# Kernel tuning notes

Hardware: AMD Instinct MI355X
Metric: run time of the kernel (lower is better)

## Reference

```python
import jax, jax.numpy as jnp
import numpy as np

EMB = 512
HEADS = 8
HEAD_DIM = EMB // HEADS


def setup_inputs() -> dict:
    key = jax.random.key(0)
    ks = jax.random.split(key, 9)
    s = 1.0 / np.sqrt(EMB)
    return {
        "x": jax.random.normal(ks[0], (4, 2048, EMB), dtype=jnp.float32),
        "Wq": jax.random.uniform(ks[1], (EMB, EMB), jnp.float32, -s, s),
        "bq": jax.random.uniform(ks[2], (EMB,), jnp.float32, -s, s),
        "Wk": jax.random.uniform(ks[3], (EMB, EMB), jnp.float32, -s, s),
        "bk": jax.random.uniform(ks[4], (EMB,), jnp.float32, -s, s),
        "Wv": jax.random.uniform(ks[5], (EMB, EMB), jnp.float32, -s, s),
        "bv": jax.random.uniform(ks[6], (EMB,), jnp.float32, -s, s),
        "Wp": jax.random.uniform(ks[7], (EMB, EMB), jnp.float32, -s, s),
        "bp": jax.random.uniform(ks[8], (EMB,), jnp.float32, -s, s),
    }


def _split_heads(t):
    b, n, _ = t.shape
    return t.reshape(b, n, HEADS, HEAD_DIM).transpose(0, 2, 1, 3)  # b h n d


def reference(x, Wq, bq, Wk, bk, Wv, bv, Wp, bp):
    q = _split_heads(x @ Wq.T + bq)
    k = _split_heads(x @ Wk.T + bk)
    v = _split_heads(x @ Wv.T + bv)
    energy = jnp.einsum("bhqd,bhkd->bhqk", q, k)
    # NOTE: original applies softmax to UNSCALED logits, then divides probs by sqrt(emb)
    att = jax.nn.softmax(energy, axis=-1) / jnp.sqrt(jnp.float32(EMB))
    out = jnp.einsum("bhqk,bhkd->bhqd", att, v)
    b, h, n, d = out.shape
    out = out.transpose(0, 2, 1, 3).reshape(b, n, h * d)
    return out @ Wp.T + bp
```

## Files before the change

kernel.cpp:

```cpp
#include <hip/hip_runtime.h>
#include <math.h>
#include <stdint.h>

#define SEQ  2048
#define LOG2E 1.4426950408889634f

typedef __attribute__((ext_vector_type(4))) float f32x4;
typedef __attribute__((ext_vector_type(16))) float f32x16;
typedef __attribute__((ext_vector_type(8))) short bf16x8;

template <int V> struct IC { static constexpr int value = V; };

__device__ __forceinline__ unsigned packbf(float a, float b) {
    return __builtin_amdgcn_perm(__float_as_uint(b) + 0x8000u,
                                 __float_as_uint(a) + 0x8000u, 0x07060302u);
}

__global__ __launch_bounds__(256, 3) void qkv_kernel(
    const float* __restrict__ xf, const float* __restrict__ wqf,
    const float* __restrict__ wkf, const float* __restrict__ wvf,
    const float* __restrict__ bq, const float* __restrict__ bk,
    const float* __restrict__ bv,
    unsigned short* __restrict__ Qw, unsigned short* __restrict__ Kw,
    unsigned short* __restrict__ VTw)
{
    __shared__ __align__(16) unsigned short smem[8192];
    unsigned short* As = smem;
    unsigned short* Bs = smem + 4096;

    const int t = threadIdx.x;
    const int w = t >> 6, lane = t & 63, quad = (t >> 4) & 3, l15 = t & 15;
    const int wr = w >> 1, wc = w & 1;
    const int m0 = blockIdx.y * 128;
    const int n0 = blockIdx.x * 128;
    const int which = n0 >> 9;
    const float* wbase = which == 0 ? wqf : (which == 1 ? wkf : wvf);
    const int nrow = n0 & 511;

    const int ar = t >> 2, akq = t & 3;
    const float* ax = xf + (size_t)(m0 + ar) * 512 + akq * 8;
    const float* bx = wbase + (size_t)(nrow + ar) * 512 + akq * 8;
    const int lws = (ar & 15) | (akq << 4);
    const int off0 = (ar >> 4) * 512 + lws * 8;
    const int off1 = off0 + 4 * 512;

    f32x4 acc[4][4];
#pragma unroll
    for (int mt = 0; mt < 4; ++mt)
#pragma unroll
        for (int nt = 0; nt < 4; ++nt) acc[mt][nt] = (f32x4){0.f, 0.f, 0.f, 0.f};

    float4 ra[4], rb[4];
    auto loadt = [&](int k0) {
        ra[0] = *(const float4*)(ax + k0);
        ra[1] = *(const float4*)(ax + k0 + 4);
        ra[2] = *(const float4*)(ax + 32768 + k0);
        ra[3] = *(const float4*)(ax + 32768 + k0 + 4);
        rb[0] = *(const float4*)(bx + k0);
        rb[1] = *(const float4*)(bx + k0 + 4);
        rb[2] = *(const float4*)(bx + 32768 + k0);
        rb[3] = *(const float4*)(bx + 32768 + k0 + 4);
    };
    auto writet = [&]() {
        uint4 p;
        p.x = packbf(ra[0].x, ra[0].y); p.y = packbf(ra[0].z, ra[0].w);
        p.z = packbf(ra[1].x, ra[1].y); p.w = packbf(ra[1].z, ra[1].w);
        *(uint4*)(As + off0) = p;
        p.x = packbf(ra[2].x, ra[2].y); p.y = packbf(ra[2].z, ra[2].w);
        p.z = packbf(ra[3].x, ra[3].y); p.w = packbf(ra[3].z, ra[3].w);
        *(uint4*)(As + off1) = p;
        p.x = packbf(rb[0].x, rb[0].y); p.y = packbf(rb[0].z, rb[0].w);
        p.z = packbf(rb[1].x, rb[1].y); p.w = packbf(rb[1].z, rb[1].w);
        *(uint4*)(Bs + off0) = p;
        p.x = packbf(rb[2].x, rb[2].y); p.y = packbf(rb[2].z, rb[2].w);
        p.z = packbf(rb[3].x, rb[3].y); p.w = packbf(rb[3].z, rb[3].w);
        *(uint4*)(Bs + off1) = p;
    };

    loadt(0);
    auto kloop = [&](auto TRC) {
        constexpr int TR = decltype(TRC)::value;
        for (int ki = 0; ki < 16; ++ki) {
            writet();
            if (ki < 15) loadt((ki + 1) * 32);
            __syncthreads();
            bf16x8 af[4], bfr[4];
#pragma unroll
            for (int mt = 0; mt < 4; ++mt)
                af[mt] = *(const bf16x8*)(As + ((wr * 4 + mt) * 64 + lane) * 8);
#pragma unroll
            for (int nt = 0; nt < 4; ++nt)
                bfr[nt] = *(const bf16x8*)(Bs + ((wc * 4 + nt) * 64 + lane) * 8);
#pragma unroll
            for (int mt = 0; mt < 4; ++mt)
#pragma unroll
                for (int nt = 0; nt < 4; ++nt) {
                    if (TR)
                        acc[mt][nt] = __builtin_amdgcn_mfma_f32_16x16x32_bf16(
                            bfr[nt], af[mt], acc[mt][nt], 0, 0, 0);
                    else
                        acc[mt][nt] = __builtin_amdgcn_mfma_f32_16x16x32_bf16(
                            af[mt], bfr[nt], acc[mt][nt], 0, 0, 0);
                }
            if (ki < 15) __syncthreads();
        }
    };
    if (which < 2) kloop(IC<1>{});
    else           kloop(IC<0>{});

    if (which == 2) {
#pragma unroll
        for (int nt = 0; nt < 4; ++nt) {
            const int n = n0 + wc * 64 + nt * 16 + l15;
            const float bias = bv[n & 511];
            const int h = (n >> 6) & 7, d = n & 63;
#pragma unroll
            for (int mt = 0; mt < 4; ++mt) {
                const int mb = m0 + wr * 64 + mt * 16 + quad * 4;
                const int bi = mb >> 11, ns = mb & 2047;
                const int bhl = bi * 8 + h;
                const f32x4 v = acc[mt][nt];
                uint2 pk;
                pk.x = packbf(v[0] + bias, v[1] + bias);
                pk.y = packbf(v[2] + bias, v[3] + bias);
                const size_t off =
                    ((size_t)(bhl * 32 + (ns >> 6)) * 8 + ((d >> 5) << 2) +
                     ((ns >> 4) & 3)) * 512 +
                    ((d & 31) << 3) + ((ns & 8) << 5) + (ns & 7);
                *(uint2*)(VTw + off) = pk;
            }
        }
    } else {
        const float sc = which ? 1.f : LOG2E;
        const float* bpt = which ? bk : bq;
        unsigned short* base = which ? Kw : Qw;
#pragma unroll
        for (int nt = 0; nt < 4; ++nt) {
            const int nb = n0 + wc * 64 + nt * 16 + quad * 4;
            const f32x4 bvv = *(const f32x4*)(bpt + (nb & 511));
            const int h = (nb >> 6) & 7, d0 = nb & 63;
#pragma unroll
            for (int mt = 0; mt < 4; ++mt) {
                const int nsg = m0 + wr * 64 + mt * 16 + l15;
                const int bi = nsg >> 11, ns = nsg & 2047;
                const int bhl = bi * 8 + h;
                const f32x4 v = acc[mt][nt];
                uint2 pk;
                pk.x = packbf((v[0] + bvv[0]) * sc, (v[1] + bvv[1]) * sc);
                pk.y = packbf((v[2] + bvv[2]) * sc, (v[3] + bvv[3]) * sc);
                const size_t off =
                    ((size_t)(bhl * 64 + (ns >> 5)) * 4 + (d0 >> 4)) * 512 +
                    ((d0 & 8) << 5) + ((ns & 31) << 3) + (d0 & 7);
                *(uint2*)(base + off) = pk;
            }
        }
    }
}

__global__ __launch_bounds__(256, 3) void outproj_kernel(
    const unsigned short* __restrict__ Aw, const float* __restrict__ wpf,
    const float* __restrict__ bp, float* __restrict__ out)
{
    __shared__ __align__(16) unsigned short smem[6144];
    unsigned short* As = smem;
    unsigned short* Bs = smem + 4096;

    const int t = threadIdx.x;
    const int w = t >> 6, lane = t & 63, quad = (t >> 4) & 3, l15 = t & 15;
    const int wr = w >> 1, wc = w & 1;
    const int m0 = blockIdx.y * 128;
    const int n0 = blockIdx.x * 64;

    const int ar = t >> 2, akq = t & 3;
    const unsigned short* ap = Aw + (size_t)(m0 + ar) * 512 + akq * 8;
    const float* bx = wpf + (size_t)(n0 + ar) * 512 + akq * 8;
    const int lws = (ar & 15) | (akq << 4);
    const int off0 = (ar >> 4) * 512 + lws * 8;
    const int off1 = off0 + 4 * 512;
    const int boff = (ar >> 4) * 512 + lws * 8;

    f32x4 acc[4][2];
#pragma unroll
    for (int mt = 0; mt < 4; ++mt)
#pragma unroll
        for (int nt = 0; nt < 2; ++nt) acc[mt][nt] = (f32x4){0.f, 0.f, 0.f, 0.f};

    uint4 ra0, ra1;
    float4 rb0, rb1;
    auto loadt = [&](int k0) {
        ra0 = *(const uint4*)(ap + k0);
        ra1 = *(const uint4*)(ap + 32768 + k0);
        rb0 = *(const float4*)(bx + k0);
        rb1 = *(const float4*)(bx + k0 + 4);
    };
    auto writet = [&]() {
        *(uint4*)(As + off0) = ra0;
        *(uint4*)(As + off1) = ra1;
        uint4 p;
        p.x = packbf(rb0.x, rb0.y); p.y = packbf(rb0.z, rb0.w);
        p.z = packbf(rb1.x, rb1.y); p.w = packbf(rb1.z, rb1.w);
        *(uint4*)(Bs + boff) = p;
    };

    loadt(0);
    for (int ki = 0; ki < 16; ++ki) {
        writet();
        if (ki < 15) loadt((ki + 1) * 32);
        __syncthreads();
        bf16x8 af[4], bfr[2];
#pragma unroll
        for (int mt = 0; mt < 4; ++mt)
            af[mt] = *(const bf16x8*)(As + ((wr * 4 + mt) * 64 + lane) * 8);
#pragma unroll
        for (int nt = 0; nt < 2; ++nt)
            bfr[nt] = *(const bf16x8*)(Bs + ((wc * 2 + nt) * 64 + lane) * 8);
#pragma unroll
        for (int mt = 0; mt < 4; ++mt)
#pragma unroll
            for (int nt = 0; nt < 2; ++nt)
                acc[mt][nt] = __builtin_amdgcn_mfma_f32_16x16x32_bf16(
                    af[mt], bfr[nt], acc[mt][nt], 0, 0, 0);
        if (ki < 15) __syncthreads();
    }

#pragma unroll
    for (int nt = 0; nt < 2; ++nt) {
        const int n = n0 + wc * 32 + nt * 16 + l15;
        const float bias = bp[n];
#pragma unroll
        for (int mt = 0; mt < 4; ++mt) {
            const int mb = m0 + wr * 64 + mt * 16 + quad * 4;
            const f32x4 v = acc[mt][nt];
#pragma unroll
            for (int r = 0; r < 4; ++r)
                out[(size_t)(mb + r) * 512 + n] = v[r] + bias;
        }
    }
}

__global__ __launch_bounds__(256, 2) void attn_kernel(
    const unsigned short* __restrict__ Qf, const unsigned short* __restrict__ Kf,
    const unsigned short* __restrict__ Vf, unsigned short* __restrict__ Ow)
{
    __shared__ float cb[8448];
    const int t = threadIdx.x;
    const int w = t >> 6, lane = t & 63;
    const int l31 = lane & 31, hlf = lane >> 5;
    const int qh = w >> 1, jh = w & 1;

    const int bh = blockIdx.x;
    const int qblk = blockIdx.y;
    const int q0 = qblk * 128;

    const unsigned short* Kp = Kf + (size_t)bh * 131072 + (jh * 4) * 512 + lane * 8;
    const unsigned short* Vp = Vf + (size_t)bh * 131072 + lane * 8;

    bf16x8 qf[2][4];
#pragma unroll
    for (int qg = 0; qg < 2; ++qg) {
        const int qgg = qblk * 4 + qh * 2 + qg;
        const unsigned short* Qp = Qf + ((size_t)(bh * 64 + qgg) * 4) * 512 + lane * 8;
#pragma unroll
        for (int kt = 0; kt < 4; ++kt)
            qf[qg][kt] = *(const bf16x8*)(Qp + kt * 512);
    }

    f32x16 zero;
#pragma unroll
    for (int r = 0; r < 16; ++r) zero[r] = 0.f;

    float lpart[2] = {0.f, 0.f};
    f32x16 Ot[2][2];
    Ot[0][0] = zero; Ot[0][1] = zero; Ot[1][0] = zero; Ot[1][1] = zero;

    bf16x8 kc[4];
#pragma unroll
    for (int c = 0; c < 4; ++c)
        kc[c] = *(const bf16x8*)(Kp + c * 512);

    for (int jt = 0; jt < 32; ++jt) {
        bf16x8 vc[4];
#pragma unroll
        for (int dg = 0; dg < 2; ++dg)
#pragma unroll
            for (int p = 0; p < 2; ++p)
                vc[dg * 2 + p] = *(const bf16x8*)(
                    Vp + (size_t)jt * 4096 + (dg * 4 + jh * 2 + p) * 512);

        f32x16 st[2];
        st[0] = zero; st[1] = zero;
#pragma unroll
        for (int kt = 0; kt < 4; ++kt) {
            st[0] = __builtin_amdgcn_mfma_f32_32x32x16_bf16(kc[kt], qf[0][kt], st[0], 0, 0, 0);
            st[1] = __builtin_amdgcn_mfma_f32_32x32x16_bf16(kc[kt], qf[1][kt], st[1], 0, 0, 0);
        }

        const int jn = (jt < 31) ? jt + 1 : 31;
#pragma unroll
        for (int c = 0; c < 4; ++c)
            kc[c] = *(const bf16x8*)(Kp + (size_t)jn * 4096 + c * 512);

#pragma unroll
        for (int qg = 0; qg < 2; ++qg) {
#pragma unroll
            for (int r = 0; r < 16; ++r)
                st[qg][r] = __builtin_amdgcn_exp2f(st[qg][r]);
            float s01 = st[qg][0] + st[qg][1],   s23 = st[qg][2] + st[qg][3];
            float s45 = st[qg][4] + st[qg][5],   s67 = st[qg][6] + st[qg][7];
            float s89 = st[qg][8] + st[qg][9],   sAB = st[qg][10] + st[qg][11];
            float sCD = st[qg][12] + st[qg][13], sEF = st[qg][14] + st[qg][15];
            lpart[qg] += ((s01 + s23) + (s45 + s67)) + ((s89 + sAB) + (sCD + sEF));
        }

        bf16x8 pf[2][2];
#pragma unroll
        for (int qg = 0; qg < 2; ++qg)
#pragma unroll
            for (int p = 0; p < 2; ++p) {
                const int r0 = p * 8;
                const unsigned a0 = packbf(st[qg][r0 + 0], st[qg][r0 + 1]);
                const unsigned a1 = packbf(st[qg][r0 + 2], st[qg][r0 + 3]);
                const unsigned b0 = packbf(st[qg][r0 + 4], st[qg][r0 + 5]);
                const unsigned b1 = packbf(st[qg][r0 + 6], st[qg][r0 + 7]);
                const unsigned ta0 = (unsigned)__shfl_xor((int)a0, 32);
                const unsigned ta1 = (unsigned)__shfl_xor((int)a1, 32);
                const unsigned tb0 = (unsigned)__shfl_xor((int)b0, 32);
                const unsigned tb1 = (unsigned)__shfl_xor((int)b1, 32);
                union { unsigned u[4]; bf16x8 v; } pb;
                pb.u[0] = hlf ? tb0 : a0;
                pb.u[1] = hlf ? tb1 : a1;
                pb.u[2] = hlf ? b0 : ta0;
                pb.u[3] = hlf ? b1 : ta1;
                pf[qg][p] = pb.v;
            }

#pragma unroll
        for (int dg = 0; dg < 2; ++dg)
#pragma unroll
            for (int p = 0; p < 2; ++p) {
                Ot[0][dg] = __builtin_amdgcn_mfma_f32_32x32x16_bf16(
                    vc[dg * 2 + p], pf[0][p], Ot[0][dg], 0, 0, 0);
                Ot[1][dg] = __builtin_amdgcn_mfma_f32_32x32x16_bf16(
                    vc[dg * 2 + p], pf[1][p], Ot[1][dg], 0, 0, 0);
            }
    }

    if (jh == 1) {
#pragma unroll
        for (int qg = 0; qg < 2; ++qg) {
#pragma unroll
            for (int dg = 0; dg < 2; ++dg) {
                const int cidx = ((qh * 2 + qg) * 2 + dg) * 4;
#pragma unroll
                for (int k = 0; k < 4; ++k) {
                    float4 v = make_float4(
                        Ot[qg][dg][k * 4 + 0], Ot[qg][dg][k * 4 + 1],
                        Ot[qg][dg][k * 4 + 2], Ot[qg][dg][k * 4 + 3]);
                    *(float4*)(cb + (cidx + k) * 256 + lane * 4) = v;
                }
            }
            cb[8192 + (qh * 2 + qg) * 64 + lane] = lpart[qg];
        }
    }
    __syncthreads();
    if (jh == 0) {
        const int bi = bh >> 3, h = bh & 7;
#pragma unroll
        for (int qg = 0; qg < 2; ++qg) {
#pragma unroll
            for (int dg = 0; dg < 2; ++dg) {
                const int cidx = ((qh * 2 + qg) * 2 + dg) * 4;
#pragma unroll
                for (int k = 0; k < 4; ++k) {
                    const float4 v = *(const float4*)(cb + (cidx + k) * 256 + lane * 4);
                    Ot[qg][dg][k * 4 + 0] += v.x;
                    Ot[qg][dg][k * 4 + 1] += v.y;
                    Ot[qg][dg][k * 4 + 2] += v.z;
                    Ot[qg][dg][k * 4 + 3] += v.w;
                }
            }
            float lv = lpart[qg] + cb[8192 + (qh * 2 + qg) * 64 + lane];
            lv += __shfl_xor(lv, 32);
            const float inv = 1.0f / (lv * 22.627416997969522f);

            const int ns = q0 + (qh * 2 + qg) * 32 + l31;
            unsigned short* dst = Ow + ((size_t)bi * SEQ + ns) * 512 + h * 64 + hlf * 4;
#pragma unroll
            for (int dg = 0; dg < 2; ++dg)
#pragma unroll
                for (int rb2 = 0; rb2 < 4; ++rb2) {
                    uint2 pk;
                    pk.x = packbf(Ot[qg][dg][rb2 * 4 + 0] * inv,
                                  Ot[qg][dg][rb2 * 4 + 1] * inv);
                    pk.y = packbf(Ot[qg][dg][rb2 * 4 + 2] * inv,
                                  Ot[qg][dg][rb2 * 4 + 3] * inv);
                    *(uint2*)(dst + dg * 32 + rb2 * 8) = pk;
                }
        }
    }
}

extern "C" void kernel_launch(void* const* d_in, const int* in_sizes, int n_in,
                              void* d_out, int out_size, void* d_ws, size_t ws_size,
                              hipStream_t stream)
{
    const float* x  = (const float*)d_in[0];
    const float* Wq = (const float*)d_in[1];
    const float* bq = (const float*)d_in[2];
    const float* Wk = (const float*)d_in[3];
    const float* bk = (const float*)d_in[4];
    const float* Wv = (const float*)d_in[5];
    const float* bv = (const float*)d_in[6];
    const float* Wp = (const float*)d_in[7];
    const float* bp = (const float*)d_in[8];

    unsigned short* ws = (unsigned short*)d_ws;
    unsigned short* Qw  = ws;
    unsigned short* Kw  = Qw + 4194304;
    unsigned short* VTw = Kw + 4194304;
    unsigned short* Owb = VTw + 4194304;

    qkv_kernel<<<dim3(12, 64), 256, 0, stream>>>(
        x, Wq, Wk, Wv, bq, bk, bv, Qw, Kw, VTw);
    attn_kernel<<<dim3(32, 16), 256, 0, stream>>>(Qw, Kw, VTw, Owb);
    outproj_kernel<<<dim3(8, 64), 256, 0, stream>>>(Owb, Wp, bp, (float*)d_out);
}
```

Measured before the change: 168.6 us.

## Split attention work across 8 waves with one query group each, add setprio

The attention kernel now runs 512 threads per block, and each wave handles a single 32-row query group instead of two. This halves per-wave accumulator and score registers and raises the wave count per CU, with launch bounds of 4 blocks per CU. Each wave now loads K/V fragments for half as much MFMA work, which doubles K/V load traffic per query. s_setprio is raised around the MFMA sections so the scheduler favours waves issuing matrix ops over those doing softmax and shuffles.

```diff
diff --git a/kernel.cpp b/kernel.cpp
--- a/kernel.cpp
+++ b/kernel.cpp
@@ -238,7 +238,7 @@
     }
 }
 
-__global__ __launch_bounds__(256, 2) void attn_kernel(
+__global__ __launch_bounds__(512, 4) void attn_kernel(
     const unsigned short* __restrict__ Qf, const unsigned short* __restrict__ Kf,
     const unsigned short* __restrict__ Vf, unsigned short* __restrict__ Ow)
 {
@@ -246,7 +246,7 @@
     const int t = threadIdx.x;
     const int w = t >> 6, lane = t & 63;
     const int l31 = lane & 31, hlf = lane >> 5;
-    const int qh = w >> 1, jh = w & 1;
+    const int qi = w >> 1, jh = w & 1;
 
     const int bh = blockIdx.x;
     const int qblk = blockIdx.y;
@@ -255,23 +255,20 @@
     const unsigned short* Kp = Kf + (size_t)bh * 131072 + (jh * 4) * 512 + lane * 8;
     const unsigned short* Vp = Vf + (size_t)bh * 131072 + lane * 8;
 
-    bf16x8 qf[2][4];
-#pragma unroll
-    for (int qg = 0; qg < 2; ++qg) {
-        const int qgg = qblk * 4 + qh * 2 + qg;
-        const unsigned short* Qp = Qf + ((size_t)(bh * 64 + qgg) * 4) * 512 + lane * 8;
-#pragma unroll
-        for (int kt = 0; kt < 4; ++kt)
-            qf[qg][kt] = *(const bf16x8*)(Qp + kt * 512);
-    }
+    const int qgg = qblk * 4 + qi;
+    const unsigned short* Qp = Qf + ((size_t)(bh * 64 + qgg) * 4) * 512 + lane * 8;
+    bf16x8 qf[4];
+#pragma unroll
+    for (int kt = 0; kt < 4; ++kt)
+        qf[kt] = *(const bf16x8*)(Qp + kt * 512);
 
     f32x16 zero;
 #pragma unroll
     for (int r = 0; r < 16; ++r) zero[r] = 0.f;
 
-    float lpart[2] = {0.f, 0.f};
-    f32x16 Ot[2][2];
-    Ot[0][0] = zero; Ot[0][1] = zero; Ot[1][0] = zero; Ot[1][1] = zero;
+    float lpart = 0.f;
+    f32x16 Ot[2];
+    Ot[0] = zero; Ot[1] = zero;
 
     bf16x8 kc[4];
 #pragma unroll
@@ -287,13 +284,12 @@
                 vc[dg * 2 + p] = *(const bf16x8*)(
                     Vp + (size_t)jt * 4096 + (dg * 4 + jh * 2 + p) * 512);
 
-        f32x16 st[2];
-        st[0] = zero; st[1] = zero;
-#pragma unroll
-        for (int kt = 0; kt < 4; ++kt) {
-            st[0] = __builtin_amdgcn_mfma_f32_32x32x16_bf16(kc[kt], qf[0][kt], st[0], 0, 0, 0);
-            st[1] = __builtin_amdgcn_mfma_f32_32x32x16_bf16(kc[kt], qf[1][kt], st[1], 0, 0, 0);
-        }
+        f32x16 st = zero;
+        __builtin_amdgcn_s_setprio(1);
+#pragma unroll
+        for (int kt = 0; kt < 4; ++kt)
+            st = __builtin_amdgcn_mfma_f32_32x32x16_bf16(kc[kt], qf[kt], st, 0, 0, 0);
+        __builtin_amdgcn_s_setprio(0);
 
         const int jn = (jt < 31) ? jt + 1 : 31;
 #pragma unroll
@@ -301,102 +297,85 @@
             kc[c] = *(const bf16x8*)(Kp + (size_t)jn * 4096 + c * 512);
 
 #pragma unroll
-        for (int qg = 0; qg < 2; ++qg) {
-#pragma unroll
-            for (int r = 0; r < 16; ++r)
-                st[qg][r] = __builtin_amdgcn_exp2f(st[qg][r]);
-            float s01 = st[qg][0] + st[qg][1],   s23 = st[qg][2] + st[qg][3];
-            float s45 = st[qg][4] + st[qg][5],   s67 = st[qg][6] + st[qg][7];
-            float s89 = st[qg][8] + st[qg][9],   sAB = st[qg][10] + st[qg][11];
-            float sCD = st[qg][12] + st[qg][13], sEF = st[qg][14] + st[qg][15];
-            lpart[qg] += ((s01 + s23) + (s45 + s67)) + ((s89 + sAB) + (sCD + sEF));
-        }
-
-        bf16x8 pf[2][2];
-#pragma unroll
-        for (int qg = 0; qg < 2; ++qg)
-#pragma unroll
-            for (int p = 0; p < 2; ++p) {
-                const int r0 = p * 8;
-                const unsigned a0 = packbf(st[qg][r0 + 0], st[qg][r0 + 1]);
-                const unsigned a1 = packbf(st[qg][r0 + 2], st[qg][r0 + 3]);
-                const unsigned b0 = packbf(st[qg][r0 + 4], st[qg][r0 + 5]);
-                const unsigned b1 = packbf(st[qg][r0 + 6], st[qg][r0 + 7]);
-                const unsigned ta0 = (unsigned)__shfl_xor((int)a0, 32);
-                const unsigned ta1 = (unsigned)__shfl_xor((int)a1, 32);
-                const unsigned tb0 = (unsigned)__shfl_xor((int)b0, 32);
-                const unsigned tb1 = (unsigned)__shfl_xor((int)b1, 32);
-                union { unsigned u[4]; bf16x8 v; } pb;
-                pb.u[0] = hlf ? tb0 : a0;
-                pb.u[1] = hlf ? tb1 : a1;
-                pb.u[2] = hlf ? b0 : ta0;
-                pb.u[3] = hlf ? b1 : ta1;
-                pf[qg][p] = pb.v;
+        for (int r = 0; r < 16; ++r)
+            st[r] = __builtin_amdgcn_exp2f(st[r]);
+        {
+            float s01 = st[0] + st[1],   s23 = st[2] + st[3];
+            float s45 = st[4] + st[5],   s67 = st[6] + st[7];
+            float s89 = st[8] + st[9],   sAB = st[10] + st[11];
+            float sCD = st[12] + st[13], sEF = st[14] + st[15];
+            lpart += ((s01 + s23) + (s45 + s67)) + ((s89 + sAB) + (sCD + sEF));
+        }
+
+#pragma unroll
+        for (int p = 0; p < 2; ++p) {
+            const int r0 = p * 8;
+            const unsigned a0 = packbf(st[r0 + 0], st[r0 + 1]);
+            const unsigned a1 = packbf(st[r0 + 2], st[r0 + 3]);
+            const unsigned b0 = packbf(st[r0 + 4], st[r0 + 5]);
+            const unsigned b1 = packbf(st[r0 + 6], st[r0 + 7]);
+            const unsigned ta0 = (unsigned)__shfl_xor((int)a0, 32);
+            const unsigned ta1 = (unsigned)__shfl_xor((int)a1, 32);
+            const unsigned tb0 = (unsigned)__shfl_xor((int)b0, 32);
+            const unsigned tb1 = (unsigned)__shfl_xor((int)b1, 32);
+            union { unsigned u[4]; bf16x8 v; } pb;
+            pb.u[0] = hlf ? tb0 : a0;
+            pb.u[1] = hlf ? tb1 : a1;
+            pb.u[2] = hlf ? b0 : ta0;
+            pb.u[3] = hlf ? b1 : ta1;
+            __builtin_amdgcn_s_setprio(1);
+            Ot[0] = __builtin_amdgcn_mfma_f32_32x32x16_bf16(vc[0 + p], pb.v, Ot[0], 0, 0, 0);
+            Ot[1] = __builtin_amdgcn_mfma_f32_32x32x16_bf16(vc[2 + p], pb.v, Ot[1], 0, 0, 0);
+            __builtin_amdgcn_s_setprio(0);
+        }
+    }
+
+    if (jh == 1) {
+#pragma unroll
+        for (int dg = 0; dg < 2; ++dg) {
+            const int cidx = (qi * 2 + dg) * 4;
+#pragma unroll
+            for (int k = 0; k < 4; ++k) {
+                float4 v = make_float4(
+                    Ot[dg][k * 4 + 0], Ot[dg][k * 4 + 1],
+                    Ot[dg][k * 4 + 2], Ot[dg][k * 4 + 3]);
+                *(float4*)(cb + (cidx + k) * 256 + lane * 4) = v;
             }
-
-#pragma unroll
-        for (int dg = 0; dg < 2; ++dg)
-#pragma unroll
-            for (int p = 0; p < 2; ++p) {
-                Ot[0][dg] = __builtin_amdgcn_mfma_f32_32x32x16_bf16(
-                    vc[dg * 2 + p], pf[0][p], Ot[0][dg], 0, 0, 0);
-                Ot[1][dg] = __builtin_amdgcn_mfma_f32_32x32x16_bf16(
-                    vc[dg * 2 + p], pf[1][p], Ot[1][dg], 0, 0, 0);
-            }
-    }
-
-    if (jh == 1) {
-#pragma unroll
-        for (int qg = 0; qg < 2; ++qg) {
-#pragma unroll
-            for (int dg = 0; dg < 2; ++dg) {
-                const int cidx = ((qh * 2 + qg) * 2 + dg) * 4;
-#pragma unroll
-                for (int k = 0; k < 4; ++k) {
-                    float4 v = make_float4(
-                        Ot[qg][dg][k * 4 + 0], Ot[qg][dg][k * 4 + 1],
-                        Ot[qg][dg][k * 4 + 2], Ot[qg][dg][k * 4 + 3]);
-                    *(float4*)(cb + (cidx + k) * 256 + lane * 4) = v;
-                }
-            }
-            cb[8192 + (qh * 2 + qg) * 64 + lane] = lpart[qg];
-        }
+        }
+        cb[8192 + qi * 64 + lane] = lpart;
     }
     __syncthreads();
     if (jh == 0) {
         const int bi = bh >> 3, h = bh & 7;
 #pragma unroll
-        for (int qg = 0; qg < 2; ++qg) {
-#pragma unroll
-            for (int dg = 0; dg < 2; ++dg) {
-                const int cidx = ((qh * 2 + qg) * 2 + dg) * 4;
-#pragma unroll
-                for (int k = 0; k < 4; ++k) {
-                    const float4 v = *(const float4*)(cb + (cidx + k) * 256 + lane * 4);
-                    Ot[qg][dg][k * 4 + 0] += v.x;
-                    Ot[qg][dg][k * 4 + 1] += v.y;
-                    Ot[qg][dg][k * 4 + 2] += v.z;
-                    Ot[qg][dg][k * 4 + 3] += v.w;
-                }
+        for (int dg = 0; dg < 2; ++dg) {
+            const int cidx = (qi * 2 + dg) * 4;
+#pragma unroll
+            for (int k = 0; k < 4; ++k) {
+                const float4 v = *(const float4*)(cb + (cidx + k) * 256 + lane * 4);
+                Ot[dg][k * 4 + 0] += v.x;
+                Ot[dg][k * 4 + 1] += v.y;
+                Ot[dg][k * 4 + 2] += v.z;
+                Ot[dg][k * 4 + 3] += v.w;
             }
-            float lv = lpart[qg] + cb[8192 + (qh * 2 + qg) * 64 + lane];
-            lv += __shfl_xor(lv, 32);
-            const float inv = 1.0f / (lv * 22.627416997969522f);
-
-            const int ns = q0 + (qh * 2 + qg) * 32 + l31;
-            unsigned short* dst = Ow + ((size_t)bi * SEQ + ns) * 512 + h * 64 + hlf * 4;
-#pragma unroll
-            for (int dg = 0; dg < 2; ++dg)
-#pragma unroll
-                for (int rb2 = 0; rb2 < 4; ++rb2) {
-                    uint2 pk;
-                    pk.x = packbf(Ot[qg][dg][rb2 * 4 + 0] * inv,
-                                  Ot[qg][dg][rb2 * 4 + 1] * inv);
-                    pk.y = packbf(Ot[qg][dg][rb2 * 4 + 2] * inv,
-                                  Ot[qg][dg][rb2 * 4 + 3] * inv);
-                    *(uint2*)(dst + dg * 32 + rb2 * 8) = pk;
-                }
-        }
+        }
+        float lv = lpart + cb[8192 + qi * 64 + lane];
+        lv += __shfl_xor(lv, 32);
+        const float inv = 1.0f / (lv * 22.627416997969522f);
+
+        const int ns = q0 + qi * 32 + l31;
+        unsigned short* dst = Ow + ((size_t)bi * SEQ + ns) * 512 + h * 64 + hlf * 4;
+#pragma unroll
+        for (int dg = 0; dg < 2; ++dg)
+#pragma unroll
+            for (int rb2 = 0; rb2 < 4; ++rb2) {
+                uint2 pk;
+                pk.x = packbf(Ot[dg][rb2 * 4 + 0] * inv,
+                              Ot[dg][rb2 * 4 + 1] * inv);
+                pk.y = packbf(Ot[dg][rb2 * 4 + 2] * inv,
+                              Ot[dg][rb2 * 4 + 3] * inv);
+                *(uint2*)(dst + dg * 32 + rb2 * 8) = pk;
+            }
     }
 }
 
@@ -422,6 +401,6 @@
 
     qkv_kernel<<<dim3(12, 64), 256, 0, stream>>>(
         x, Wq, Wk, Wv, bq, bk, bv, Qw, Kw, VTw);
-    attn_kernel<<<dim3(32, 16), 256, 0, stream>>>(Qw, Kw, VTw, Owb);
+    attn_kernel<<<dim3(32, 16), 512, 0, stream>>>(Qw, Kw, VTw, Owb);
     outproj_kernel<<<dim3(8, 64), 256, 0, stream>>>(Owb, Wp, bp, (float*)d_out);
 }
```

After: 173.0 us. +2.7%, slower.
